# Kernel optimization log

Measured on AMD Instinct MI355X. Metric: run time of the kernel, lower is better.

Reference implementation:

```python
import jax, jax.numpy as jnp
import numpy as np

HID = 128      # hidden_dim
CDIM = 128     # c_dim
NBLK = 5       # n_blocks
RESO = 32      # grid_resolution
G = RESO ** 3  # number of voxels
B, T = 2, 100000


def setup_inputs() -> dict:
    key = jax.random.key(0)
    ks = jax.random.split(key, 8)
    return {
        "points": jax.random.normal(ks[0], (B, T, 3), jnp.float32),
        "index": jax.random.randint(ks[1], (B, 1, T), 0, G, dtype=jnp.int64),
        # fc_pos: Linear(3, 2*HID)
        "fc_pos_w": jax.random.normal(ks[2], (3, 2 * HID), jnp.float32) * 0.1,
        "fc_pos_b": jnp.zeros((2 * HID,), jnp.float32),
        # ResnetBlockFC(2*HID, HID) x NBLK: fc_0 (2H->H), fc_1 (H->H), shortcut (2H->H, no bias)
        "fc0_w": jax.random.normal(ks[3], (NBLK, 2 * HID, HID), jnp.float32) * 0.05,
        "fc0_b": jnp.zeros((NBLK, HID), jnp.float32),
        "fc1_w": jax.random.normal(ks[4], (NBLK, HID, HID), jnp.float32) * 0.05,
        "fc1_b": jnp.zeros((NBLK, HID), jnp.float32),
        "sc_w": jax.random.normal(ks[5], (NBLK, 2 * HID, HID), jnp.float32) * 0.05,
        # fc_c: Linear(HID, CDIM)
        "fc_c_w": jax.random.normal(ks[6], (HID, CDIM), jnp.float32) * 0.05,
        "fc_c_b": jnp.zeros((CDIM,), jnp.float32),
    }


def _resnet_block(x, w0, b0, w1, b1, ws):
    # ResnetBlockFC: net = fc_0(relu(x)); dx = fc_1(relu(net)); out = shortcut(x) + dx
    net = jnp.maximum(x, 0.0) @ w0 + b0
    dx = jnp.maximum(net, 0.0) @ w1 + b1
    return x @ ws + dx


def reference(points, index, fc_pos_w, fc_pos_b, fc0_w, fc0_b, fc1_w, fc1_b, sc_w, fc_c_w, fc_c_b):
    idx = index[:, 0, :]  # [B, T]

    def pool_local(net):
        # scatter_max over voxels, then gather back per point
        seg = jax.vmap(lambda c_b, i_b: jax.ops.segment_max(c_b, i_b, num_segments=G))(net, idx)  # [B,G,H]
        return jnp.take_along_axis(seg, idx[:, :, None], axis=1)  # [B,T,H]; every gathered voxel is non-empty

    net = points @ fc_pos_w + fc_pos_b          # [B,T,2H]
    net = _resnet_block(net, fc0_w[0], fc0_b[0], fc1_w[0], fc1_b[0], sc_w[0])  # [B,T,H]
    for i in range(1, NBLK):
        pooled = pool_local(net)
        net = jnp.concatenate([net, pooled], axis=2)  # [B,T,2H]
        net = _resnet_block(net, fc0_w[i], fc0_b[i], fc1_w[i], fc1_b[i], sc_w[i])

    c = net @ fc_c_w + fc_c_b  # [B,T,CDIM]

    # generate_grid_features: scatter_mean into the 32^3 grid (zeros for empty voxels)
    sums = jax.vmap(lambda c_b, i_b: jax.ops.segment_sum(c_b, i_b, num_segments=G))(c, idx)  # [B,G,CDIM]
    cnts = jax.vmap(lambda i_b: jax.ops.segment_sum(jnp.ones((T,), c.dtype), i_b, num_segments=G))(idx)  # [B,G]
    cnts = cnts[:, :, None]
    mean = jnp.where(cnts > 0, sums / jnp.maximum(cnts, 1.0), 0.0)
    fea_grid = jnp.transpose(mean, (0, 2, 1)).reshape(B, CDIM, RESO, RESO, RESO)
    return fea_grid
```

## Files before the change

kernel.cpp:

```cpp
#include <hip/hip_runtime.h>

#define T_PTS 100000
#define NB 2
#define GCELLS 32768
#define NCELL (NB * GCELLS)
#define HID 128
#define MBLK 64
#define RBPB 1563
#define GRID_RB (NB * RBPB)

typedef __attribute__((ext_vector_type(8))) short bf16x8;
typedef __attribute__((ext_vector_type(4))) float f32x4;

#define MFMA16 __builtin_amdgcn_mfma_f32_16x16x32_bf16

__device__ __forceinline__ unsigned short bf16rne(float f) {
  unsigned u = __float_as_uint(f);
  return (unsigned short)((u + 0x7FFFu + ((u >> 16) & 1u)) >> 16);
}
__device__ __forceinline__ unsigned packhl(float f) {
  unsigned short h = bf16rne(f);
  float hf = __uint_as_float(((unsigned)h) << 16);
  unsigned short l = bf16rne(f - hf);
  return (((unsigned)h) << 16) | (unsigned)l;
}

union U8 { bf16x8 v; unsigned u[4]; };

__device__ __forceinline__ void up2(unsigned w0, unsigned w1, unsigned& h,
                                    unsigned& l) {
  h = __builtin_amdgcn_perm(w1, w0, 0x07060302u);
  l = __builtin_amdgcn_perm(w1, w0, 0x05040100u);
}

template <int MODE>
__global__ __launch_bounds__(256, 3) void resblock_mfma(
    const void* __restrict__ srcv, const float* __restrict__ posw,
    const float* __restrict__ posb, const unsigned* __restrict__ cell,
    const int* __restrict__ idx, const unsigned short* __restrict__ w0p,
    const float* __restrict__ b0, const unsigned short* __restrict__ w1p,
    const float* __restrict__ b1, const unsigned short* __restrict__ swp,
    unsigned* __restrict__ net_out) {
  __shared__ unsigned lds32[8192];
  const int tid = threadIdx.x;
  const int lane = tid & 63;
  const int wid = tid >> 6;
  const int wc = wid;
  const int b = blockIdx.x / RBPB;
  const int t0 = (blockIdx.x % RBPB) * MBLK;
  const int valid = (T_PTS - t0 < MBLK) ? (T_PTS - t0) : MBLK;

  const int pt = tid >> 2;
  const int kc = (tid & 3) << 3;
  const int ptc = (t0 + pt < T_PTS) ? pt : (T_PTS - 1 - t0);
  const unsigned* nrow = nullptr;
  const unsigned* crow = nullptr;
  float pp0 = 0.f, pp1 = 0.f, pp2 = 0.f;
  if (MODE == 1) {
    const long prow = (long)b * T_PTS + t0 + ptc;
    nrow = (const unsigned*)srcv + prow * HID;
    crow = cell + ((long)b * GCELLS + idx[prow]) * HID;
  } else {
    const float* ppp = (const float*)srcv + ((long)b * T_PTS + t0 + ptc) * 3;
    pp0 = ppp[0]; pp1 = ppp[1]; pp2 = ppp[2];
  }

  auto load_x = [&](int ks, unsigned* w) {
    if (MODE == 1) {
      const unsigned* rp = (ks < 4) ? (nrow + ks * 32 + kc)
                                    : (crow + (ks - 4) * 32 + kc);
      uint4 a = *(const uint4*)rp;
      uint4 c = *(const uint4*)(rp + 4);
      w[0] = a.x; w[1] = a.y; w[2] = a.z; w[3] = a.w;
      w[4] = c.x; w[5] = c.y; w[6] = c.z; w[7] = c.w;
    } else {
      const int kb = ks * 32 + kc;
      float xv[8];
#pragma unroll
      for (int i = 0; i < 8; i += 4) {
        float4 wa = *(const float4*)(posw + kb + i);
        float4 wb = *(const float4*)(posw + 256 + kb + i);
        float4 wcc = *(const float4*)(posw + 512 + kb + i);
        float4 bb = *(const float4*)(posb + kb + i);
        xv[i + 0] = fmaf(pp0, wa.x, fmaf(pp1, wb.x, fmaf(pp2, wcc.x, bb.x)));
        xv[i + 1] = fmaf(pp0, wa.y, fmaf(pp1, wb.y, fmaf(pp2, wcc.y, bb.y)));
        xv[i + 2] = fmaf(pp0, wa.z, fmaf(pp1, wb.z, fmaf(pp2, wcc.z, bb.z)));
        xv[i + 3] = fmaf(pp0, wa.w, fmaf(pp1, wb.w, fmaf(pp2, wcc.w, bb.w)));
      }
#pragma unroll
      for (int i = 0; i < 8; ++i) w[i] = packhl(xv[i]);
    }
  };

  auto store_x = [&](int ks, const unsigned* w) {
    unsigned* p = &lds32[((ks & 1) << 11) + wid * 512 + lane * 4];
    uint4 q;
    q.x = w[0]; q.y = w[1]; q.z = w[2]; q.w = w[3];
    *(uint4*)p = q;
    q.x = w[4]; q.y = w[5]; q.z = w[6]; q.w = w[7];
    *(uint4*)(p + 256) = q;
  };

  auto load_B = [&](const unsigned short* base, int loOff, int ks, bf16x8* h,
                    bf16x8* l) {
#pragma unroll
    for (int nt = 0; nt < 2; ++nt) {
      const int fi = (ks * 8 + wc * 2 + nt) * 512 + lane * 8;
      h[nt] = *(const bf16x8*)(base + fi);
      l[nt] = *(const bf16x8*)(base + loOff + fi);
    }
  };

  f32x4 accy[4][2], acco[4][2];
#pragma unroll
  for (int i = 0; i < 4; ++i)
#pragma unroll
    for (int j = 0; j < 2; ++j) {
      f32x4 z = {0.f, 0.f, 0.f, 0.f};
      accy[i][j] = z;
      acco[i][j] = z;
    }

  {
    unsigned w[8];
    load_x(0, w);
    store_x(0, w);
  }
  __syncthreads();

  const int lam = (lane & 15) * 4 + (lane >> 4);
#pragma unroll 1
  for (int ks = 0; ks < 8; ++ks) {
    bf16x8 b1h[2], b1l[2], b2h[2], b2l[2];
    load_B(w0p, 32768, ks, b1h, b1l);
    load_B(swp, 32768, ks, b2h, b2l);
    unsigned nxt[8];
    if (ks < 7) load_x(ks + 1, nxt);
    const int sb = (ks & 1) << 11;
    __builtin_amdgcn_s_setprio(1);
#pragma unroll
    for (int mt = 0; mt < 4; ++mt) {
      const unsigned* p = &lds32[sb + mt * 512 + lam * 4];
      uint4 q1 = *(const uint4*)p;
      uint4 q2 = *(const uint4*)(p + 256);
      unsigned q[8] = {q1.x, q1.y, q1.z, q1.w, q2.x, q2.y, q2.z, q2.w};
      U8 xh, xl, rh, rl;
#pragma unroll
      for (int p2 = 0; p2 < 4; ++p2) {
        const unsigned w0 = q[2 * p2], w1 = q[2 * p2 + 1];
        const unsigned r0 = ((int)w0 < 0) ? 0u : w0;
        const unsigned r1 = ((int)w1 < 0) ? 0u : w1;
        up2(w0, w1, xh.u[p2], xl.u[p2]);
        up2(r0, r1, rh.u[p2], rl.u[p2]);
      }
#pragma unroll
      for (int nt = 0; nt < 2; ++nt) {
        accy[mt][nt] = MFMA16(rh.v, b1h[nt], accy[mt][nt], 0, 0, 0);
        accy[mt][nt] = MFMA16(rh.v, b1l[nt], accy[mt][nt], 0, 0, 0);
        accy[mt][nt] = MFMA16(rl.v, b1h[nt], accy[mt][nt], 0, 0, 0);
      }
#pragma unroll
      for (int nt = 0; nt < 2; ++nt) {
        acco[mt][nt] = MFMA16(xh.v, b2h[nt], acco[mt][nt], 0, 0, 0);
        acco[mt][nt] = MFMA16(xh.v, b2l[nt], acco[mt][nt], 0, 0, 0);
        acco[mt][nt] = MFMA16(xl.v, b2h[nt], acco[mt][nt], 0, 0, 0);
      }
    }
    __builtin_amdgcn_s_setprio(0);
    if (ks < 7) store_x(ks + 1, nxt);
    __syncthreads();
  }

  {
    float b0v[2];
#pragma unroll
    for (int nt = 0; nt < 2; ++nt)
      b0v[nt] = b0[wc * 32 + nt * 16 + (lane & 15)];
#pragma unroll
    for (int mt = 0; mt < 4; ++mt) {
#pragma unroll
      for (int nt = 0; nt < 2; ++nt) {
        const int c = wc * 32 + nt * 16 + (lane & 15);
        const int k2 = c >> 5;
        const int j = c & 7;
        const int lahi = ((c & 31) >> 3) * 16;
#pragma unroll
        for (int r = 0; r < 4; ++r) {
          float h = fmaxf(accy[mt][nt][r] + b0v[nt], 0.f);
          int la = lahi + (lane >> 4) * 4 + r;
          la ^= (la >> 3) & 7;
          lds32[((k2 * 4 + mt) * 64 + la) * 8 + j] = packhl(h);
        }
      }
    }
  }
  __syncthreads();

  {
    const int lar2 = lane ^ ((lane >> 3) & 7);
#pragma unroll
    for (int k2 = 0; k2 < 4; ++k2) {
      bf16x8 ch[2], cl[2];
      load_B(w1p, 16384, k2, ch, cl);
      __builtin_amdgcn_s_setprio(1);
#pragma unroll
      for (int mt = 0; mt < 4; ++mt) {
        const unsigned* p = &lds32[((k2 * 4 + mt) * 64 + lar2) * 8];
        uint4 q1 = *(const uint4*)p;
        uint4 q2 = *(const uint4*)(p + 4);
        unsigned q[8] = {q1.x, q1.y, q1.z, q1.w, q2.x, q2.y, q2.z, q2.w};
        U8 ah, al;
#pragma unroll
        for (int p2 = 0; p2 < 4; ++p2)
          up2(q[2 * p2], q[2 * p2 + 1], ah.u[p2], al.u[p2]);
#pragma unroll
        for (int nt = 0; nt < 2; ++nt) {
          acco[mt][nt] = MFMA16(ah.v, ch[nt], acco[mt][nt], 0, 0, 0);
          acco[mt][nt] = MFMA16(ah.v, cl[nt], acco[mt][nt], 0, 0, 0);
          acco[mt][nt] = MFMA16(al.v, ch[nt], acco[mt][nt], 0, 0, 0);
        }
      }
      __builtin_amdgcn_s_setprio(0);
    }
  }

  {
    float b1v[2];
#pragma unroll
    for (int nt = 0; nt < 2; ++nt)
      b1v[nt] = b1[wc * 32 + nt * 16 + (lane & 15)];
#pragma unroll
    for (int mt = 0; mt < 4; ++mt) {
#pragma unroll
      for (int r = 0; r < 4; ++r) {
        const int row = mt * 16 + (lane >> 4) * 4 + r;
        if (row < valid) {
          unsigned* op = net_out + ((long)b * T_PTS + t0 + row) * HID;
          op[wc * 32 + (lane & 15)] = packhl(acco[mt][0][r] + b1v[0]);
          op[wc * 32 + 16 + (lane & 15)] = packhl(acco[mt][1][r] + b1v[1]);
        }
      }
    }
  }
}

__global__ __launch_bounds__(256, 4) void final_mfma(
    unsigned* __restrict__ net, const unsigned short* __restrict__ wcp,
    const float* __restrict__ bc) {
  __shared__ unsigned lds32[4096];
  const int tid = threadIdx.x;
  const int lane = tid & 63;
  const int wid = tid >> 6;
  const int wc = wid;
  const int b = blockIdx.x / RBPB;
  const int t0 = (blockIdx.x % RBPB) * MBLK;
  const int valid = (T_PTS - t0 < MBLK) ? (T_PTS - t0) : MBLK;

  const int pt = tid >> 2;
  const int kc = (tid & 3) << 3;
  const int ptc = (t0 + pt < T_PTS) ? pt : (T_PTS - 1 - t0);
  const unsigned* nrow = net + ((long)b * T_PTS + t0 + ptc) * HID;

  auto load_x = [&](int ks, unsigned* w) {
    const unsigned* rp = nrow + ks * 32 + kc;
    uint4 a = *(const uint4*)rp;
    uint4 c = *(const uint4*)(rp + 4);
    w[0] = a.x; w[1] = a.y; w[2] = a.z; w[3] = a.w;
    w[4] = c.x; w[5] = c.y; w[6] = c.z; w[7] = c.w;
  };
  auto store_x = [&](int ks, const unsigned* w) {
    unsigned* p = &lds32[((ks & 1) << 11) + wid * 512 + lane * 4];
    uint4 q;
    q.x = w[0]; q.y = w[1]; q.z = w[2]; q.w = w[3];
    *(uint4*)p = q;
    q.x = w[4]; q.y = w[5]; q.z = w[6]; q.w = w[7];
    *(uint4*)(p + 256) = q;
  };
  auto load_B = [&](int ks, bf16x8* h, bf16x8* l) {
#pragma unroll
    for (int nt = 0; nt < 2; ++nt) {
      const int fi = (ks * 8 + wc * 2 + nt) * 512 + lane * 8;
      h[nt] = *(const bf16x8*)(wcp + fi);
      l[nt] = *(const bf16x8*)(wcp + 16384 + fi);
    }
  };

  f32x4 acc[4][2];
#pragma unroll
  for (int i = 0; i < 4; ++i)
#pragma unroll
    for (int j = 0; j < 2; ++j) {
      f32x4 z = {0.f, 0.f, 0.f, 0.f};
      acc[i][j] = z;
    }

  {
    unsigned w[8];
    load_x(0, w);
    store_x(0, w);
  }
  __syncthreads();

  const int lam = (lane & 15) * 4 + (lane >> 4);
#pragma unroll 1
  for (int ks = 0; ks < 4; ++ks) {
    bf16x8 ch[2], cl[2];
    load_B(ks, ch, cl);
    unsigned nxt[8];
    if (ks < 3) load_x(ks + 1, nxt);
    const int sb = (ks & 1) << 11;
    __builtin_amdgcn_s_setprio(1);
#pragma unroll
    for (int mt = 0; mt < 4; ++mt) {
      const unsigned* p = &lds32[sb + mt * 512 + lam * 4];
      uint4 q1 = *(const uint4*)p;
      uint4 q2 = *(const uint4*)(p + 256);
      unsigned q[8] = {q1.x, q1.y, q1.z, q1.w, q2.x, q2.y, q2.z, q2.w};
      U8 ah, al;
#pragma unroll
      for (int p2 = 0; p2 < 4; ++p2)
        up2(q[2 * p2], q[2 * p2 + 1], ah.u[p2], al.u[p2]);
#pragma unroll
      for (int nt = 0; nt < 2; ++nt) {
        acc[mt][nt] = MFMA16(ah.v, ch[nt], acc[mt][nt], 0, 0, 0);
        acc[mt][nt] = MFMA16(ah.v, cl[nt], acc[mt][nt], 0, 0, 0);
        acc[mt][nt] = MFMA16(al.v, ch[nt], acc[mt][nt], 0, 0, 0);
      }
    }
    __builtin_amdgcn_s_setprio(0);
    if (ks < 3) store_x(ks + 1, nxt);
    __syncthreads();
  }

  float* fout = (float*)net;
  float bcv[2];
#pragma unroll
  for (int nt = 0; nt < 2; ++nt)
    bcv[nt] = bc[wc * 32 + nt * 16 + (lane & 15)];
#pragma unroll
  for (int mt = 0; mt < 4; ++mt) {
#pragma unroll
    for (int r = 0; r < 4; ++r) {
      const int row = mt * 16 + (lane >> 4) * 4 + r;
      if (row < valid) {
        float* op = fout + ((long)b * T_PTS + t0 + row) * HID;
        op[wc * 32 + (lane & 15)] = acc[mt][0][r] + bcv[0];
        op[wc * 32 + 16 + (lane & 15)] = acc[mt][1][r] + bcv[1];
      }
    }
  }
}

__global__ void pack_weights(const float* __restrict__ fc0,
                             const float* __restrict__ fc1,
                             const float* __restrict__ sc,
                             const float* __restrict__ fcc,
                             unsigned short* __restrict__ w0p,
                             unsigned short* __restrict__ w1p,
                             unsigned short* __restrict__ swp,
                             unsigned short* __restrict__ wcp) {
  int gid = blockIdx.x * 256 + threadIdx.x;
  const float* src;
  unsigned short* dst;
  int K, e;
  if (gid < 163840) { src = fc0; dst = w0p; K = 256; e = gid; }
  else if (gid < 327680) { src = sc; dst = swp; K = 256; e = gid - 163840; }
  else if (gid < 409600) { src = fc1; dst = w1p; K = 128; e = gid - 327680; }
  else if (gid < 425984) { src = fcc; dst = wcp; K = 128; e = gid - 409600; }
  else return;
  const int mat = e / (K * 128);
  const int r = e - mat * K * 128;
  const int k = r >> 7, n = r & 127;
  const float x = src[e];
  const unsigned short hi = bf16rne(x);
  const float hf = __uint_as_float(((unsigned)hi) << 16);
  const unsigned short lo = bf16rne(x - hf);
  const int ks = k >> 5, lg = (k >> 3) & 3, j = k & 7;
  const int l = lg * 16 + (n & 15), nt = n >> 4;
  unsigned short* mb = dst + (long)mat * K * 256;
  const int off = ((ks * 8 + nt) * 64 + l) * 8 + j;
  mb[off] = hi;
  mb[off + K * 128] = lo;
}

__global__ void zero_i32(int* __restrict__ p, int n) {
  const int i = blockIdx.x * 256 + threadIdx.x;
  if (i < n) p[i] = 0;
}

__global__ void count_csr(const int* __restrict__ idx, int* __restrict__ curs) {
  const int gid = blockIdx.x * 256 + threadIdx.x;
  if (gid >= NB * T_PTS) return;
  const int b = gid / T_PTS;
  atomicAdd(&curs[b * GCELLS + idx[gid]], 1);
}

__global__ __launch_bounds__(1024) void scan_csr(const int* __restrict__ cnt,
                                                 int* __restrict__ offsets) {
  __shared__ int part[1024];
  const int t = threadIdx.x;
  const int base = t * (NCELL / 1024);
  int s = 0;
  for (int i = 0; i < NCELL / 1024; ++i) s += cnt[base + i];
  part[t] = s;
  __syncthreads();
  for (int d = 1; d < 1024; d <<= 1) {
    int v = (t >= d) ? part[t - d] : 0;
    __syncthreads();
    part[t] += v;
    __syncthreads();
  }
  int run = (t == 0) ? 0 : part[t - 1];
  for (int i = 0; i < NCELL / 1024; ++i) {
    offsets[base + i] = run;
    run += cnt[base + i];
  }
  if (t == 1023) offsets[NCELL] = run;
}

__global__ void scatter_csr(const int* __restrict__ idx,
                            const int* __restrict__ offsets,
                            int* __restrict__ curs, int* __restrict__ perm) {
  const int gid = blockIdx.x * 256 + threadIdx.x;
  if (gid >= NB * T_PTS) return;
  const int b = gid / T_PTS;
  const int cellk = b * GCELLS + idx[gid];
  const int slot = offsets[cellk] + atomicAdd(&curs[cellk], 1);
  perm[slot] = gid;
}

__global__ __launch_bounds__(256) void pool_csr(const unsigned* __restrict__ net,
                                                const int* __restrict__ perm,
                                                const int* __restrict__ offsets,
                                                unsigned* __restrict__ cellf) {
  const int cellk = blockIdx.x * 4 + (threadIdx.x >> 6);
  const int lane = threadIdx.x & 63;
  const int s0 = offsets[cellk], s1 = offsets[cellk + 1];
  if (s0 >= s1) return;
  float m0 = -3.402823466e38f, m1 = -3.402823466e38f;
  unsigned b0 = 0u, b1 = 0u;
  for (int j = s0; j < s1; ++j) {
    const long row = perm[j];
    uint2 w = *(const uint2*)(net + row * HID + lane * 2);
    float v0 = __uint_as_float(w.x & 0xFFFF0000u) + __uint_as_float(w.x << 16);
    float v1 = __uint_as_float(w.y & 0xFFFF0000u) + __uint_as_float(w.y << 16);
    if (v0 > m0) { m0 = v0; b0 = w.x; }
    if (v1 > m1) { m1 = v1; b1 = w.y; }
  }
  uint2 o; o.x = b0; o.y = b1;
  *(uint2*)(cellf + (long)cellk * HID + lane * 2) = o;
}

__global__ __launch_bounds__(256) void cellsum_csr(
    const float* __restrict__ c, const int* __restrict__ perm,
    const int* __restrict__ offsets, float* __restrict__ sums) {
  const int cellk = blockIdx.x * 4 + (threadIdx.x >> 6);
  const int lane = threadIdx.x & 63;
  const int s0 = offsets[cellk], s1 = offsets[cellk + 1];
  if (s0 >= s1) return;
  float2 m = {0.f, 0.f};
  for (int j = s0; j < s1; ++j) {
    const long row = perm[j];
    float2 v = *(const float2*)(c + row * HID + lane * 2);
    m.x += v.x;
    m.y += v.y;
  }
  *(float2*)(sums + (long)cellk * HID + lane * 2) = m;
}

__global__ void mean_kernel(const float* __restrict__ sums,
                            const int* __restrict__ offsets,
                            float* __restrict__ out) {
  const long gid = (long)blockIdx.x * 256 + threadIdx.x;
  if (gid >= (long)NB * HID * GCELLS) return;
  const int g = (int)(gid % GCELLS);
  const int c = (int)((gid / GCELLS) % HID);
  const int b = (int)(gid / ((long)HID * GCELLS));
  const int cellk = b * GCELLS + g;
  const int cnt = offsets[cellk + 1] - offsets[cellk];
  out[gid] = cnt > 0 ? sums[(long)cellk * HID + c] / (float)cnt : 0.f;
}

extern "C" void kernel_launch(void* const* d_in, const int* in_sizes, int n_in,
                              void* d_out, int out_size, void* d_ws,
                              size_t ws_size, hipStream_t stream) {
  const float* points = (const float*)d_in[0];
  const int* idx = (const int*)d_in[1];
  const float* fc_pos_w = (const float*)d_in[2];
  const float* fc_pos_b = (const float*)d_in[3];
  const float* fc0_w = (const float*)d_in[4];
  const float* fc0_b = (const float*)d_in[5];
  const float* fc1_w = (const float*)d_in[6];
  const float* fc1_b = (const float*)d_in[7];
  const float* sc_w = (const float*)d_in[8];
  const float* fc_c_w = (const float*)d_in[9];
  const float* fc_c_b = (const float*)d_in[10];
  float* out = (float*)d_out;

  const long NET_BYTES = (long)NB * T_PTS * HID * 4;
  const long CELL_BYTES = (long)NB * GCELLS * HID * 4;
  unsigned* net = (unsigned*)d_ws;
  unsigned* cellf = (unsigned*)((char*)d_ws + NET_BYTES);
  float* sums = (float*)cellf;
  int* offsets = (int*)((char*)d_ws + NET_BYTES + CELL_BYTES);

  unsigned short* packs = (unsigned short*)d_out;
  unsigned short* w0p = packs;
  unsigned short* swp = packs + 327680;
  unsigned short* w1p = packs + 655360;
  unsigned short* wcp = packs + 819200;
  int* curs = (int*)((char*)d_out + (2l << 20));
  int* perm = (int*)((char*)d_out + (3l << 20));

  const int GRID_PTS = (NB * T_PTS + 255) / 256;
  const int GRID_ZERO = (NCELL + 255) / 256;
  const int GRID_CELL = NCELL / 4;
  const int GRID_MEAN = NB * HID * GCELLS / 256;

  pack_weights<<<1664, 256, 0, stream>>>(fc0_w, fc1_w, sc_w, fc_c_w, w0p, w1p,
                                         swp, wcp);

  zero_i32<<<GRID_ZERO, 256, 0, stream>>>(curs, NCELL);
  count_csr<<<GRID_PTS, 256, 0, stream>>>(idx, curs);
  scan_csr<<<1, 1024, 0, stream>>>(curs, offsets);
  zero_i32<<<GRID_ZERO, 256, 0, stream>>>(curs, NCELL);
  scatter_csr<<<GRID_PTS, 256, 0, stream>>>(idx, offsets, curs, perm);

  resblock_mfma<0><<<GRID_RB, 256, 0, stream>>>(
      points, fc_pos_w, fc_pos_b, nullptr, nullptr, w0p, fc0_b, w1p, fc1_b,
      swp, net);

  for (int i = 1; i < 5; ++i) {
    pool_csr<<<GRID_CELL, 256, 0, stream>>>(net, perm, offsets, cellf);
    resblock_mfma<1><<<GRID_RB, 256, 0, stream>>>(
        net, nullptr, nullptr, cellf, idx, w0p + (long)i * 65536,
        fc0_b + i * HID, w1p + (long)i * 32768, fc1_b + i * HID,
        swp + (long)i * 65536, net);
  }

  final_mfma<<<GRID_RB, 256, 0, stream>>>(net, wcp, fc_c_b);
  cellsum_csr<<<GRID_CELL, 256, 0, stream>>>((const float*)net, perm, offsets,
                                             sums);
  mean_kernel<<<GRID_MEAN, 256, 0, stream>>>(sums, offsets, out);
}
```

Measured before the change: 800.6 us.

## Stage activation tiles via direct global-to-LDS loads and split weight loads

Replaces the register round-trip (global load into VGPRs, then LDS store) for activation tiles with global_load_lds DMA writes straight into LDS, remapping the staging rows so each lane's layout matches the MFMA read pattern directly. The resblock inner loop is split into two phases that load the fc0 and shortcut weight fragments in turn, cutting live B-fragment registers. Together these free VGPRs so the launch bound is raised from 3 to 4 blocks per SM. The risk is that DMA completion is ordered only by the existing barriers, and the compiler may not insert the right waits.

```diff
diff --git a/kernel.cpp b/kernel.cpp
--- a/kernel.cpp
+++ b/kernel.cpp
@@ -33,8 +33,14 @@
   l = __builtin_amdgcn_perm(w1, w0, 0x05040100u);
 }
 
+__device__ __forceinline__ void dma16(const unsigned* g, unsigned* l) {
+  __builtin_amdgcn_global_load_lds(
+      (const __attribute__((address_space(1))) unsigned*)g,
+      (__attribute__((address_space(3))) unsigned*)l, 16, 0, 0);
+}
+
 template <int MODE>
-__global__ __launch_bounds__(256, 3) void resblock_mfma(
+__global__ __launch_bounds__(256, 4) void resblock_mfma(
     const void* __restrict__ srcv, const float* __restrict__ posw,
     const float* __restrict__ posb, const unsigned* __restrict__ cell,
     const int* __restrict__ idx, const unsigned short* __restrict__ w0p,
@@ -50,31 +56,30 @@
   const int t0 = (blockIdx.x % RBPB) * MBLK;
   const int valid = (T_PTS - t0 < MBLK) ? (T_PTS - t0) : MBLK;
 
-  const int pt = tid >> 2;
-  const int kc = (tid & 3) << 3;
-  const int ptc = (t0 + pt < T_PTS) ? pt : (T_PTS - 1 - t0);
-  const unsigned* nrow = nullptr;
-  const unsigned* crow = nullptr;
+  const int srow = wid * 16 + (lane & 15);
+  const int skc = (lane >> 4) * 8;
+  const int ptc = (t0 + srow < T_PTS) ? srow : (T_PTS - 1 - t0);
+  const unsigned* nrowL = nullptr;
+  const unsigned* crowL = nullptr;
   float pp0 = 0.f, pp1 = 0.f, pp2 = 0.f;
   if (MODE == 1) {
     const long prow = (long)b * T_PTS + t0 + ptc;
-    nrow = (const unsigned*)srcv + prow * HID;
-    crow = cell + ((long)b * GCELLS + idx[prow]) * HID;
+    nrowL = (const unsigned*)srcv + prow * HID;
+    crowL = cell + ((long)b * GCELLS + idx[prow]) * HID;
   } else {
     const float* ppp = (const float*)srcv + ((long)b * T_PTS + t0 + ptc) * 3;
     pp0 = ppp[0]; pp1 = ppp[1]; pp2 = ppp[2];
   }
 
-  auto load_x = [&](int ks, unsigned* w) {
+  auto stage = [&](int ks) {
+    unsigned* base = &lds32[(ks & 1) * 2048 + wid * 512];
     if (MODE == 1) {
-      const unsigned* rp = (ks < 4) ? (nrow + ks * 32 + kc)
-                                    : (crow + (ks - 4) * 32 + kc);
-      uint4 a = *(const uint4*)rp;
-      uint4 c = *(const uint4*)(rp + 4);
-      w[0] = a.x; w[1] = a.y; w[2] = a.z; w[3] = a.w;
-      w[4] = c.x; w[5] = c.y; w[6] = c.z; w[7] = c.w;
+      const unsigned* rp =
+          ((ks < 4) ? nrowL + ks * 32 : crowL + (ks - 4) * 32) + skc;
+      dma16(rp, base);
+      dma16(rp + 4, base + 256);
     } else {
-      const int kb = ks * 32 + kc;
+      const int kb = ks * 32 + skc;
       float xv[8];
 #pragma unroll
       for (int i = 0; i < 8; i += 4) {
@@ -87,18 +92,16 @@
         xv[i + 2] = fmaf(pp0, wa.z, fmaf(pp1, wb.z, fmaf(pp2, wcc.z, bb.z)));
         xv[i + 3] = fmaf(pp0, wa.w, fmaf(pp1, wb.w, fmaf(pp2, wcc.w, bb.w)));
       }
+      unsigned w[8];
 #pragma unroll
       for (int i = 0; i < 8; ++i) w[i] = packhl(xv[i]);
-    }
-  };
-
-  auto store_x = [&](int ks, const unsigned* w) {
-    unsigned* p = &lds32[((ks & 1) << 11) + wid * 512 + lane * 4];
-    uint4 q;
-    q.x = w[0]; q.y = w[1]; q.z = w[2]; q.w = w[3];
-    *(uint4*)p = q;
-    q.x = w[4]; q.y = w[5]; q.z = w[6]; q.w = w[7];
-    *(uint4*)(p + 256) = q;
+      unsigned* p = base + lane * 4;
+      uint4 q;
+      q.x = w[0]; q.y = w[1]; q.z = w[2]; q.w = w[3];
+      *(uint4*)p = q;
+      q.x = w[4]; q.y = w[5]; q.z = w[6]; q.w = w[7];
+      *(uint4*)(p + 256) = q;
+    }
   };
 
   auto load_B = [&](const unsigned short* base, int loOff, int ks, bf16x8* h,
@@ -121,53 +124,59 @@
       acco[i][j] = z;
     }
 
-  {
-    unsigned w[8];
-    load_x(0, w);
-    store_x(0, w);
-  }
+  stage(0);
   __syncthreads();
 
-  const int lam = (lane & 15) * 4 + (lane >> 4);
 #pragma unroll 1
   for (int ks = 0; ks < 8; ++ks) {
-    bf16x8 b1h[2], b1l[2], b2h[2], b2l[2];
-    load_B(w0p, 32768, ks, b1h, b1l);
-    load_B(swp, 32768, ks, b2h, b2l);
-    unsigned nxt[8];
-    if (ks < 7) load_x(ks + 1, nxt);
     const int sb = (ks & 1) << 11;
+    bf16x8 bh[2], bl[2];
+    load_B(w0p, 32768, ks, bh, bl);
+    if (ks < 7) stage(ks + 1);
     __builtin_amdgcn_s_setprio(1);
 #pragma unroll
     for (int mt = 0; mt < 4; ++mt) {
-      const unsigned* p = &lds32[sb + mt * 512 + lam * 4];
+      const unsigned* p = &lds32[sb + mt * 512 + lane * 4];
       uint4 q1 = *(const uint4*)p;
       uint4 q2 = *(const uint4*)(p + 256);
       unsigned q[8] = {q1.x, q1.y, q1.z, q1.w, q2.x, q2.y, q2.z, q2.w};
-      U8 xh, xl, rh, rl;
+      U8 rh, rl;
 #pragma unroll
       for (int p2 = 0; p2 < 4; ++p2) {
         const unsigned w0 = q[2 * p2], w1 = q[2 * p2 + 1];
         const unsigned r0 = ((int)w0 < 0) ? 0u : w0;
         const unsigned r1 = ((int)w1 < 0) ? 0u : w1;
-        up2(w0, w1, xh.u[p2], xl.u[p2]);
         up2(r0, r1, rh.u[p2], rl.u[p2]);
       }
 #pragma unroll
       for (int nt = 0; nt < 2; ++nt) {
-        accy[mt][nt] = MFMA16(rh.v, b1h[nt], accy[mt][nt], 0, 0, 0);
-        accy[mt][nt] = MFMA16(rh.v, b1l[nt], accy[mt][nt], 0, 0, 0);
-        accy[mt][nt] = MFMA16(rl.v, b1h[nt], accy[mt][nt], 0, 0, 0);
-      }
+        accy[mt][nt] = MFMA16(rh.v, bh[nt], accy[mt][nt], 0, 0, 0);
+        accy[mt][nt] = MFMA16(rh.v, bl[nt], accy[mt][nt], 0, 0, 0);
+        accy[mt][nt] = MFMA16(rl.v, bh[nt], accy[mt][nt], 0, 0, 0);
+      }
+    }
+    __builtin_amdgcn_s_setprio(0);
+    asm volatile("" ::: "memory");
+    load_B(swp, 32768, ks, bh, bl);
+    __builtin_amdgcn_s_setprio(1);
+#pragma unroll
+    for (int mt = 0; mt < 4; ++mt) {
+      const unsigned* p = &lds32[sb + mt * 512 + lane * 4];
+      uint4 q1 = *(const uint4*)p;
+      uint4 q2 = *(const uint4*)(p + 256);
+      unsigned q[8] = {q1.x, q1.y, q1.z, q1.w, q2.x, q2.y, q2.z, q2.w};
+      U8 xh, xl;
+#pragma unroll
+      for (int p2 = 0; p2 < 4; ++p2)
+        up2(q[2 * p2], q[2 * p2 + 1], xh.u[p2], xl.u[p2]);
 #pragma unroll
       for (int nt = 0; nt < 2; ++nt) {
-        acco[mt][nt] = MFMA16(xh.v, b2h[nt], acco[mt][nt], 0, 0, 0);
-        acco[mt][nt] = MFMA16(xh.v, b2l[nt], acco[mt][nt], 0, 0, 0);
-        acco[mt][nt] = MFMA16(xl.v, b2h[nt], acco[mt][nt], 0, 0, 0);
+        acco[mt][nt] = MFMA16(xh.v, bh[nt], acco[mt][nt], 0, 0, 0);
+        acco[mt][nt] = MFMA16(xh.v, bl[nt], acco[mt][nt], 0, 0, 0);
+        acco[mt][nt] = MFMA16(xl.v, bh[nt], acco[mt][nt], 0, 0, 0);
       }
     }
     __builtin_amdgcn_s_setprio(0);
-    if (ks < 7) store_x(ks + 1, nxt);
     __syncthreads();
   }
 
@@ -256,25 +265,16 @@
   const int t0 = (blockIdx.x % RBPB) * MBLK;
   const int valid = (T_PTS - t0 < MBLK) ? (T_PTS - t0) : MBLK;
 
-  const int pt = tid >> 2;
-  const int kc = (tid & 3) << 3;
-  const int ptc = (t0 + pt < T_PTS) ? pt : (T_PTS - 1 - t0);
-  const unsigned* nrow = net + ((long)b * T_PTS + t0 + ptc) * HID;
-
-  auto load_x = [&](int ks, unsigned* w) {
-    const unsigned* rp = nrow + ks * 32 + kc;
-    uint4 a = *(const uint4*)rp;
-    uint4 c = *(const uint4*)(rp + 4);
-    w[0] = a.x; w[1] = a.y; w[2] = a.z; w[3] = a.w;
-    w[4] = c.x; w[5] = c.y; w[6] = c.z; w[7] = c.w;
-  };
-  auto store_x = [&](int ks, const unsigned* w) {
-    unsigned* p = &lds32[((ks & 1) << 11) + wid * 512 + lane * 4];
-    uint4 q;
-    q.x = w[0]; q.y = w[1]; q.z = w[2]; q.w = w[3];
-    *(uint4*)p = q;
-    q.x = w[4]; q.y = w[5]; q.z = w[6]; q.w = w[7];
-    *(uint4*)(p + 256) = q;
+  const int srow = wid * 16 + (lane & 15);
+  const int skc = (lane >> 4) * 8;
+  const int ptc = (t0 + srow < T_PTS) ? srow : (T_PTS - 1 - t0);
+  const unsigned* nrowL = net + ((long)b * T_PTS + t0 + ptc) * HID;
+
+  auto stage = [&](int ks) {
+    unsigned* base = &lds32[(ks & 1) * 2048 + wid * 512];
+    const unsigned* rp = nrowL + ks * 32 + skc;
+    dma16(rp, base);
+    dma16(rp + 4, base + 256);
   };
   auto load_B = [&](int ks, bf16x8* h, bf16x8* l) {
 #pragma unroll
@@ -294,25 +294,19 @@
       acc[i][j] = z;
     }
 
-  {
-    unsigned w[8];
-    load_x(0, w);
-    store_x(0, w);
-  }
+  stage(0);
   __syncthreads();
 
-  const int lam = (lane & 15) * 4 + (lane >> 4);
 #pragma unroll 1
   for (int ks = 0; ks < 4; ++ks) {
+    const int sb = (ks & 1) << 11;
     bf16x8 ch[2], cl[2];
     load_B(ks, ch, cl);
-    unsigned nxt[8];
-    if (ks < 3) load_x(ks + 1, nxt);
-    const int sb = (ks & 1) << 11;
+    if (ks < 3) stage(ks + 1);
     __builtin_amdgcn_s_setprio(1);
 #pragma unroll
     for (int mt = 0; mt < 4; ++mt) {
-      const unsigned* p = &lds32[sb + mt * 512 + lam * 4];
+      const unsigned* p = &lds32[sb + mt * 512 + lane * 4];
       uint4 q1 = *(const uint4*)p;
       uint4 q2 = *(const uint4*)(p + 256);
       unsigned q[8] = {q1.x, q1.y, q1.z, q1.w, q2.x, q2.y, q2.z, q2.w};
@@ -328,7 +322,6 @@
       }
     }
     __builtin_amdgcn_s_setprio(0);
-    if (ks < 3) store_x(ks + 1, nxt);
     __syncthreads();
   }
 
```

Measured after the change: 801.3 us. Within noise of the previous version (+0.1%).
